# Performance work log

Hardware: AMD Instinct MI355X
Metric: run time of the kernel (lower is better)

## Reference

```python
import jax, jax.numpy as jnp
import numpy as np

B, DIM, T, H = 8, 1024, 2048, 16
HD = DIM // H  # per-head channel dim = 64


def _toeplitz(v):
    # v: (H, T) -> (H, T, T) with M[h, i, j] = v[h, j - i] if j >= i else 0
    m = v.shape[-1]
    i = jnp.arange(m)[:, None]
    j = jnp.arange(m)[None, :]
    idx = jnp.where(j >= i, j - i, 0)
    return jnp.where(j >= i, v[..., idx], jnp.zeros((), v.dtype))


def setup_inputs() -> dict:
    key = jax.random.key(0)
    ks = jax.random.split(key, 5)
    s = 1.0 / np.sqrt(DIM)
    return {
        "x": jax.random.normal(ks[0], (B, DIM, T), jnp.float32),
        "w_in": jax.random.normal(ks[1], (DIM, DIM), jnp.float32) * s,
        "b_in": jnp.zeros((DIM,), jnp.float32),
        "w_out": jax.random.normal(ks[2], (DIM, DIM), jnp.float32) * s,
        "b_out": jnp.zeros((DIM,), jnp.float32),
        "toep_w": jax.random.normal(ks[3], (H, T), jnp.float32) * 0.02,
        "toep_b": jnp.zeros((H, T), jnp.float32),
    }


def reference(x, w_in, b_in, w_out, b_out, toep_w, toep_b):
    # x: (B, DIM, T) -> (B, T, DIM)
    xt = jnp.transpose(x, (0, 2, 1))
    h1 = xt @ w_in.T + b_in  # (B, T, DIM)
    # (B, T, H*HD) -> (B, H, HD, T)
    p = jnp.transpose(h1.reshape(B, T, H, HD), (0, 2, 3, 1))
    M = _toeplitz(toep_w)  # (H, T, T)
    # bmm with per-head causal Toeplitz matrix + per-head bias over time
    conv = jnp.einsum("bhdt,htu->bhdu", p, M) + toep_b[None, :, None, :]
    # (B, H, HD, T) -> (B, T, H*HD)
    merged = jnp.transpose(conv, (0, 3, 1, 2)).reshape(B, T, DIM)
    out = merged @ w_out.T + b_out  # (B, T, DIM)
    return jnp.transpose(out, (0, 2, 1))  # (B, DIM, T)
```

## Files before the change

kernel.cpp:

```cpp
#include <hip/hip_runtime.h>
#include <hip/hip_bf16.h>
#include <stdint.h>

#define B_   8
#define DIM  1024
#define T_   2048
#define H_   16
#define HD   64

typedef __attribute__((ext_vector_type(8))) short bf16x8;
typedef __attribute__((ext_vector_type(4))) float f32x4;

__device__ __forceinline__ unsigned short f2bf(float f) {
    union { float f; unsigned u; } v{f};
    unsigned r = v.u + 0x7fffu + ((v.u >> 16) & 1u);
    return (unsigned short)(r >> 16);
}

__device__ __forceinline__ void gl_lds16(const unsigned short* g, unsigned short* l) {
    __builtin_amdgcn_global_load_lds(
        (const __attribute__((address_space(1))) void*)(const void*)g,
        (__attribute__((address_space(3))) void*)(void*)l,
        16, 0, 0);
}

__device__ __forceinline__ bf16x8 ld_frag(const unsigned short* smem, int row, int cg) {
    return *reinterpret_cast<const bf16x8*>(smem + row * 64 + (((cg) ^ (row & 7)) << 3));
}

__global__ void xpose_cast(const float* __restrict__ x, unsigned short* __restrict__ xt) {
    __shared__ float tile[64][65];
    const int b = blockIdx.z;
    const int d0 = blockIdx.y * 64, t0 = blockIdx.x * 64;
    const int tid = threadIdx.x;
    const int c = tid & 63;
    const int r0 = tid >> 6;

    const float* xp = x + ((size_t)b * DIM + d0) * T_ + t0;
#pragma unroll
    for (int i = 0; i < 16; ++i) {
        int r = r0 + i * 4;
        tile[r][c] = xp[(size_t)r * T_ + c];
    }
    __syncthreads();
    unsigned short* op = xt + ((size_t)b * T_ + t0) * DIM + d0;
#pragma unroll
    for (int i = 0; i < 16; ++i) {
        int r = r0 + i * 4;
        op[(size_t)r * DIM + c] = f2bf(tile[c][r]);
    }
}

__global__ void cast_weights(const float* __restrict__ w_in, const float* __restrict__ w_out,
                             const float* __restrict__ tw,
                             unsigned short* __restrict__ w_in_b, unsigned short* __restrict__ w_out_b,
                             unsigned short* __restrict__ tw_b) {
    int i = blockIdx.x * 256 + threadIdx.x;
    if (i < DIM * DIM) {
        w_in_b[i]  = f2bf(w_in[i]);
        w_out_b[i] = f2bf(w_out[i]);
    }
    if (i < H_ * T_) tw_b[i] = f2bf(tw[i]);
}

__global__ void gen_mdiag(const unsigned short* __restrict__ twb, unsigned short* __restrict__ Md) {
    const int h = blockIdx.y, dg = blockIdx.x;
    const int D = (dg - 1) * 64;
    unsigned short* out = Md + (((size_t)h * 32 + dg) << 13);
    for (int v = threadIdx.x; v < 1024; v += 256) {
        int u = v >> 3, j0 = (v & 7) * 8;
        bf16x8 w;
#pragma unroll
        for (int j = 0; j < 8; ++j) {
            int lag = D + u - (j0 + j);
            w[j] = (lag >= 0) ? (short)twb[h * T_ + lag] : (short)0;
        }
        *reinterpret_cast<bf16x8*>(out + v * 8) = w;
    }
}

template <bool OUT_BF16>
__global__ void gemm_k(const unsigned short* __restrict__ Aw,
                       const unsigned short* __restrict__ Bm,
                       const float* __restrict__ bias,
                       void* __restrict__ Out) {
    __shared__ __align__(16) unsigned short As[128 * 64];
    __shared__ __align__(16) unsigned short Bs[128 * 64];

    const int tid = threadIdx.x, lane = tid & 63, wv = tid >> 6;
    const int b = blockIdx.z;
    const int m0 = blockIdx.y * 128;
    const int n0 = blockIdx.x * 128;
    const unsigned short* Bb = Bm + (size_t)b * T_ * DIM;

    const int wr = wv >> 1, wc = wv & 1;
    const int lrow = lane & 15, lg = lane >> 4;

    f32x4 acc[4][4] = {};

    for (int k0 = 0; k0 < DIM; k0 += 64) {
        __syncthreads();
#pragma unroll
        for (int it = 0; it < 4; ++it) {
            int ch = wv * 4 + it;
            int r  = ch * 8 + (lane >> 3);
            int g  = (lane & 7) ^ (lane >> 3);
            gl_lds16(Aw + (size_t)(m0 + r) * DIM + k0 + g * 8, As + ch * 512);
            gl_lds16(Bb + (size_t)(n0 + r) * DIM + k0 + g * 8, Bs + ch * 512);
        }
        __syncthreads();

#pragma unroll
        for (int kk = 0; kk < 2; ++kk) {
            bf16x8 af[4], bfr[4];
#pragma unroll
            for (int mt = 0; mt < 4; ++mt) af[mt]  = ld_frag(As, wr * 64 + mt * 16 + lrow, kk * 4 + lg);
#pragma unroll
            for (int nt = 0; nt < 4; ++nt) bfr[nt] = ld_frag(Bs, wc * 64 + nt * 16 + lrow, kk * 4 + lg);
#pragma unroll
            for (int mt = 0; mt < 4; ++mt)
#pragma unroll
                for (int nt = 0; nt < 4; ++nt)
                    acc[mt][nt] = __builtin_amdgcn_mfma_f32_16x16x32_bf16(af[mt], bfr[nt], acc[mt][nt], 0, 0, 0);
        }
    }

    const size_t ob = (size_t)b * DIM * T_;
#pragma unroll
    for (int mt = 0; mt < 4; ++mt) {
        int d = m0 + wr * 64 + mt * 16 + lg * 4;
#pragma unroll
        for (int nt = 0; nt < 4; ++nt) {
            int t = n0 + wc * 64 + nt * 16 + lrow;
#pragma unroll
            for (int r = 0; r < 4; ++r) {
                float v = acc[mt][nt][r] + bias[d + r];
                if constexpr (OUT_BF16)
                    ((unsigned short*)Out)[ob + (size_t)(d + r) * T_ + t] = f2bf(v);
                else
                    ((float*)Out)[ob + (size_t)(d + r) * T_ + t] = v;
            }
        }
    }
}

__global__ void conv3_k(const unsigned short* __restrict__ H1,
                        const unsigned short* __restrict__ Md,
                        const float* __restrict__ tb,
                        unsigned short* __restrict__ Cb) {
    __shared__ __align__(16) unsigned short As[128 * 64];
    __shared__ __align__(16) unsigned short Ps[64 * 64];

    const int tid = threadIdx.x, lane = tid & 63, wv = tid >> 6;
    const int h = blockIdx.y;
    const int b = blockIdx.z;
    const unsigned short* Hb = H1 + ((size_t)b * DIM + h * HD) * T_;

    const int lrow = lane & 15, lg = lane >> 4;
    const int rsub = lane >> 3;
    const int g = (lane & 7) ^ rsub;

#pragma unroll
    for (int ph = 0; ph < 2; ++ph) {
        const int ut = ph ? blockIdx.x : (T_ / 128 - 1 - blockIdx.x);
        const int u0 = ut * 128;
        f32x4 acc[2][4] = {};

        const int nk = 2 * ut + 2;
        for (int kt = 0; kt < nk; ++kt) {
            const int t0 = kt * 64;
            const int dg = 2 * ut - kt + 1;
            const unsigned short* At = Md + (((size_t)h * 32 + dg) << 13);
            __syncthreads();
#pragma unroll
            for (int it = 0; it < 4; ++it) {
                int ch = wv * 4 + it;
                int r  = ch * 8 + rsub;
                gl_lds16(At + (size_t)r * 64 + g * 8, As + ch * 512);
            }
#pragma unroll
            for (int it = 0; it < 2; ++it) {
                int ch = wv * 2 + it;
                int r  = ch * 8 + rsub;
                gl_lds16(Hb + (size_t)r * T_ + t0 + g * 8, Ps + ch * 512);
            }
            __syncthreads();

#pragma unroll
            for (int kk = 0; kk < 2; ++kk) {
                bf16x8 af[2], bfr[4];
#pragma unroll
                for (int mt = 0; mt < 2; ++mt) af[mt]  = ld_frag(As, wv * 32 + mt * 16 + lrow, kk * 4 + lg);
#pragma unroll
                for (int nt = 0; nt < 4; ++nt) bfr[nt] = ld_frag(Ps, nt * 16 + lrow, kk * 4 + lg);
#pragma unroll
                for (int mt = 0; mt < 2; ++mt)
#pragma unroll
                    for (int nt = 0; nt < 4; ++nt)
                        acc[mt][nt] = __builtin_amdgcn_mfma_f32_16x16x32_bf16(af[mt], bfr[nt], acc[mt][nt], 0, 0, 0);
            }
        }

        const size_t base = (size_t)b * T_ * DIM + (size_t)h * HD;
#pragma unroll
        for (int mt = 0; mt < 2; ++mt) {
            int u = u0 + wv * 32 + mt * 16 + lg * 4;
            const float* tbp = tb + h * T_ + u;
            float t0v = tbp[0], t1v = tbp[1], t2v = tbp[2], t3v = tbp[3];
#pragma unroll
            for (int nt = 0; nt < 4; ++nt) {
                int d = nt * 16 + lrow;
                size_t p = base + (size_t)u * DIM + d;
                Cb[p]           = f2bf(acc[mt][nt][0] + t0v);
                Cb[p + DIM]     = f2bf(acc[mt][nt][1] + t1v);
                Cb[p + 2 * DIM] = f2bf(acc[mt][nt][2] + t2v);
                Cb[p + 3 * DIM] = f2bf(acc[mt][nt][3] + t3v);
            }
        }
    }
}

extern "C" void kernel_launch(void* const* d_in, const int* in_sizes, int n_in,
                              void* d_out, int out_size, void* d_ws, size_t ws_size,
                              hipStream_t stream) {
    (void)in_sizes; (void)n_in; (void)out_size; (void)ws_size;
    const float* x      = (const float*)d_in[0];
    const float* w_in   = (const float*)d_in[1];
    const float* b_in   = (const float*)d_in[2];
    const float* w_out  = (const float*)d_in[3];
    const float* b_out  = (const float*)d_in[4];
    const float* toep_w = (const float*)d_in[5];
    const float* toep_b = (const float*)d_in[6];

    char* ws = (char*)d_ws;
    unsigned short* XT    = (unsigned short*)(ws);
    unsigned short* H1    = (unsigned short*)(ws + 33554432);
    unsigned short* Cbuf  = (unsigned short*)(ws + 67108864);
    unsigned short* winb  = (unsigned short*)(ws + 100663296);
    unsigned short* woutb = (unsigned short*)(ws + 102760448);
    unsigned short* twb   = (unsigned short*)(ws + 104857600);
    unsigned short* Mdiag = (unsigned short*)(ws + 104923136);

    xpose_cast<<<dim3(T_ / 64, DIM / 64, B_), dim3(256), 0, stream>>>(x, XT);
    cast_weights<<<dim3((DIM * DIM) / 256), dim3(256), 0, stream>>>(w_in, w_out, toep_w, winb, woutb, twb);
    gen_mdiag<<<dim3(32, H_), dim3(256), 0, stream>>>(twb, Mdiag);
    gemm_k<true><<<dim3(T_ / 128, DIM / 128, B_), dim3(256), 0, stream>>>(winb, XT, b_in, (void*)H1);
    conv3_k<<<dim3(T_ / 256, H_, B_), dim3(256), 0, stream>>>(H1, Mdiag, toep_b, Cbuf);
    gemm_k<false><<<dim3(T_ / 128, DIM / 128, B_), dim3(256), 0, stream>>>(woutb, Cbuf, b_out, d_out);
}
```

Before: 174.3 us.

## Pre-layout Toeplitz tiles as MFMA fragments, double-buffer P, remap grid for XCD locality

The Toeplitz diagonal blocks are now generated directly in MFMA fragment order, so the conv kernel loads A operands straight from global memory into registers instead of staging them through LDS. The P tile is double-buffered so the next tile's load overlaps compute, which leaves one barrier per iteration. All three GEMM-style kernels now use a flat 1D grid remapped so that consecutive blocks on the same XCD share weights and heads, aiming for better L2 reuse. The cost is direct global loads of A fragments, which depend on cache hits.

```diff
diff --git a/kernel.cpp b/kernel.cpp
--- a/kernel.cpp
+++ b/kernel.cpp
@@ -63,19 +63,19 @@
     if (i < H_ * T_) tw_b[i] = f2bf(tw[i]);
 }
 
-__global__ void gen_mdiag(const unsigned short* __restrict__ twb, unsigned short* __restrict__ Md) {
+__global__ void gen_mfrag(const unsigned short* __restrict__ twb, unsigned short* __restrict__ Mf) {
     const int h = blockIdx.y, dg = blockIdx.x;
     const int D = (dg - 1) * 64;
-    unsigned short* out = Md + (((size_t)h * 32 + dg) << 13);
+    unsigned short* out = Mf + (((size_t)h * 32 + dg) << 13);
     for (int v = threadIdx.x; v < 1024; v += 256) {
-        int u = v >> 3, j0 = (v & 7) * 8;
+        int cg = v >> 7, row = v & 127;
         bf16x8 w;
 #pragma unroll
         for (int j = 0; j < 8; ++j) {
-            int lag = D + u - (j0 + j);
+            int lag = D + row - (cg * 8 + j);
             w[j] = (lag >= 0) ? (short)twb[h * T_ + lag] : (short)0;
         }
-        *reinterpret_cast<bf16x8*>(out + v * 8) = w;
+        *reinterpret_cast<bf16x8*>(out + (size_t)v * 8) = w;
     }
 }
 
@@ -87,10 +87,15 @@
     __shared__ __align__(16) unsigned short As[128 * 64];
     __shared__ __align__(16) unsigned short Bs[128 * 64];
 
+    const int flat = blockIdx.x;
+    const int wid  = (flat & 7) * 128 + (flat >> 3);
+    const int nx   = wid & 15;
+    const int my   = (wid >> 4) & 7;
+    const int b    = wid >> 7;
+
     const int tid = threadIdx.x, lane = tid & 63, wv = tid >> 6;
-    const int b = blockIdx.z;
-    const int m0 = blockIdx.y * 128;
-    const int n0 = blockIdx.x * 128;
+    const int m0 = my * 128;
+    const int n0 = nx * 128;
     const unsigned short* Bb = Bm + (size_t)b * T_ * DIM;
 
     const int wr = wv >> 1, wc = wv & 1;
@@ -144,61 +149,80 @@
     }
 }
 
-__global__ void conv3_k(const unsigned short* __restrict__ H1,
-                        const unsigned short* __restrict__ Md,
+__global__ void conv4_k(const unsigned short* __restrict__ H1,
+                        const unsigned short* __restrict__ Mf,
                         const float* __restrict__ tb,
                         unsigned short* __restrict__ Cb) {
-    __shared__ __align__(16) unsigned short As[128 * 64];
-    __shared__ __align__(16) unsigned short Ps[64 * 64];
+    __shared__ __align__(16) unsigned short Ps[2][64 * 64];
+
+    const int flat = blockIdx.x;
+    const int wid  = (flat & 7) * 128 + (flat >> 3);
+    const int bx   = wid & 7;
+    const int b    = (wid >> 3) & 7;
+    const int h    = wid >> 6;
 
     const int tid = threadIdx.x, lane = tid & 63, wv = tid >> 6;
-    const int h = blockIdx.y;
-    const int b = blockIdx.z;
     const unsigned short* Hb = H1 + ((size_t)b * DIM + h * HD) * T_;
+    const unsigned short* Ah = Mf + ((size_t)h * 32) * 8192;
 
     const int lrow = lane & 15, lg = lane >> 4;
     const int rsub = lane >> 3;
     const int g = (lane & 7) ^ rsub;
 
+    const int aoff = (lg * 128 + wv * 32 + lrow) * 8;
+
 #pragma unroll
     for (int ph = 0; ph < 2; ++ph) {
-        const int ut = ph ? blockIdx.x : (T_ / 128 - 1 - blockIdx.x);
+        const int ut = ph ? bx : (T_ / 128 - 1 - bx);
         const int u0 = ut * 128;
+        const int nk = 2 * ut + 2;
         f32x4 acc[2][4] = {};
 
-        const int nk = 2 * ut + 2;
+#pragma unroll
+        for (int it = 0; it < 2; ++it) {
+            int ch = wv * 2 + it;
+            int r  = ch * 8 + rsub;
+            gl_lds16(Hb + (size_t)r * T_ + g * 8, &Ps[0][0] + ch * 512);
+        }
+        __syncthreads();
+
         for (int kt = 0; kt < nk; ++kt) {
-            const int t0 = kt * 64;
+            const int cur = kt & 1;
+            if (kt + 1 < nk) {
+                const int t0n = (kt + 1) * 64;
+#pragma unroll
+                for (int it = 0; it < 2; ++it) {
+                    int ch = wv * 2 + it;
+                    int r  = ch * 8 + rsub;
+                    gl_lds16(Hb + (size_t)r * T_ + t0n + g * 8, &Ps[cur ^ 1][0] + ch * 512);
+                }
+            }
             const int dg = 2 * ut - kt + 1;
-            const unsigned short* At = Md + (((size_t)h * 32 + dg) << 13);
+            const unsigned short* At = Ah + (size_t)dg * 8192;
+            bf16x8 af0[2], af1[2];
+#pragma unroll
+            for (int mt = 0; mt < 2; ++mt) {
+                af0[mt] = *reinterpret_cast<const bf16x8*>(At + aoff + mt * 128);
+                af1[mt] = *reinterpret_cast<const bf16x8*>(At + 4096 + aoff + mt * 128);
+            }
+            const unsigned short* Pb = &Ps[cur][0];
+            bf16x8 bfr[4];
+#pragma unroll
+            for (int nt = 0; nt < 4; ++nt) bfr[nt] = ld_frag(Pb, nt * 16 + lrow, lg);
+#pragma unroll
+            for (int mt = 0; mt < 2; ++mt)
+#pragma unroll
+                for (int nt = 0; nt < 4; ++nt)
+                    acc[mt][nt] = __builtin_amdgcn_mfma_f32_16x16x32_bf16(af0[mt], bfr[nt], acc[mt][nt], 0, 0, 0);
+#pragma unroll
+            for (int nt = 0; nt < 4; ++nt) bfr[nt] = ld_frag(Pb, nt * 16 + lrow, 4 + lg);
+#pragma unroll
+            for (int mt = 0; mt < 2; ++mt)
+#pragma unroll
+                for (int nt = 0; nt < 4; ++nt)
+                    acc[mt][nt] = __builtin_amdgcn_mfma_f32_16x16x32_bf16(af1[mt], bfr[nt], acc[mt][nt], 0, 0, 0);
+
             __syncthreads();
-#pragma unroll
-            for (int it = 0; it < 4; ++it) {
-                int ch = wv * 4 + it;
-                int r  = ch * 8 + rsub;
-                gl_lds16(At + (size_t)r * 64 + g * 8, As + ch * 512);
-            }
-#pragma unroll
-            for (int it = 0; it < 2; ++it) {
-                int ch = wv * 2 + it;
-                int r  = ch * 8 + rsub;
-                gl_lds16(Hb + (size_t)r * T_ + t0 + g * 8, Ps + ch * 512);
-            }
-            __syncthreads();
-
-#pragma unroll
-            for (int kk = 0; kk < 2; ++kk) {
-                bf16x8 af[2], bfr[4];
-#pragma unroll
-                for (int mt = 0; mt < 2; ++mt) af[mt]  = ld_frag(As, wv * 32 + mt * 16 + lrow, kk * 4 + lg);
-#pragma unroll
-                for (int nt = 0; nt < 4; ++nt) bfr[nt] = ld_frag(Ps, nt * 16 + lrow, kk * 4 + lg);
-#pragma unroll
-                for (int mt = 0; mt < 2; ++mt)
-#pragma unroll
-                    for (int nt = 0; nt < 4; ++nt)
-                        acc[mt][nt] = __builtin_amdgcn_mfma_f32_16x16x32_bf16(af[mt], bfr[nt], acc[mt][nt], 0, 0, 0);
-            }
         }
 
         const size_t base = (size_t)b * T_ * DIM + (size_t)h * HD;
@@ -239,12 +263,12 @@
     unsigned short* winb  = (unsigned short*)(ws + 100663296);
     unsigned short* woutb = (unsigned short*)(ws + 102760448);
     unsigned short* twb   = (unsigned short*)(ws + 104857600);
-    unsigned short* Mdiag = (unsigned short*)(ws + 104923136);
+    unsigned short* Mfrag = (unsigned short*)(ws + 104923136);
 
     xpose_cast<<<dim3(T_ / 64, DIM / 64, B_), dim3(256), 0, stream>>>(x, XT);
     cast_weights<<<dim3((DIM * DIM) / 256), dim3(256), 0, stream>>>(w_in, w_out, toep_w, winb, woutb, twb);
-    gen_mdiag<<<dim3(32, H_), dim3(256), 0, stream>>>(twb, Mdiag);
-    gemm_k<true><<<dim3(T_ / 128, DIM / 128, B_), dim3(256), 0, stream>>>(winb, XT, b_in, (void*)H1);
-    conv3_k<<<dim3(T_ / 256, H_, B_), dim3(256), 0, stream>>>(H1, Mdiag, toep_b, Cbuf);
-    gemm_k<false><<<dim3(T_ / 128, DIM / 128, B_), dim3(256), 0, stream>>>(woutb, Cbuf, b_out, d_out);
-}
+    gen_mfrag<<<dim3(32, H_), dim3(256), 0, stream>>>(twb, Mfrag);
+    gemm_k<true><<<dim3(1024), dim3(256), 0, stream>>>(winb, XT, b_in, (void*)H1);
+    conv4_k<<<dim3(1024), dim3(256), 0, stream>>>(H1, Mfrag, toep_b, Cbuf);
+    gemm_k<false><<<dim3(1024), dim3(256), 0, stream>>>(woutb, Cbuf, b_out, d_out);
+}
```

After: 145.3 us. -16.7%, faster.
